# Kernel tuning notes

Hardware: AMD Instinct MI355X
Metric: run time of the kernel (lower is better)

The kernel has to match this reference:

```python
import jax, jax.numpy as jnp
import numpy as np

B, S, DIM, EXTRA, NK, NH, NL = 16, 256, 41, 1, 128, 4, 3
ND = DIM + EXTRA  # 42 channels after appending the Time2Vec extra channel


def _lin(key, fin, fout):
    kw, kb = jax.random.split(key)
    w = jax.random.normal(kw, (fin, fout), jnp.float32) / np.float32(np.sqrt(fin))
    b = jax.random.normal(kb, (fout,), jnp.float32) * 0.01
    return w, b


def _stack(key, fin, fout):
    ws, bs = zip(*[_lin(k, fin, fout) for k in jax.random.split(key, NL)])
    return jnp.stack(ws), jnp.stack(bs)


def setup_inputs():
    key = jax.random.key(0)
    ks = jax.random.split(key, 32)
    inp = {}
    inp['context_x'] = jnp.sort(jax.random.uniform(ks[0], (B, S), jnp.float32), axis=1)
    inp['value'] = jax.random.normal(ks[1], (B, S, DIM), jnp.float32)
    mask = (jax.random.uniform(ks[2], (B, S, DIM)) < 0.23).astype(jnp.float32)
    inp['mask'] = mask
    inp['target_value'] = jax.random.normal(ks[3], (B, S, DIM), jnp.float32)
    inp['target_mask'] = mask * (jax.random.uniform(ks[4], (B, S, DIM)) < 0.3).astype(jnp.float32)
    inp['t2v_w0'] = jax.random.normal(ks[5], (1,), jnp.float32)
    inp['t2v_b0'] = jax.random.normal(ks[6], (1,), jnp.float32)
    inp['edge_w'], inp['edge_b'] = _lin(ks[7], 2, NK)
    inp['chan_w'], inp['chan_b'] = _lin(ks[8], ND, NK)
    inp['time_w'], inp['time_b'] = _lin(ks[9], 1, NK)
    base = 10
    for pre, dk in (('ct', 2 * NK), ('tc', 2 * NK), ('ca', NK)):
        inp[pre + '_wq'], inp[pre + '_bq'] = _stack(ks[base], NK, NK); base += 1
        inp[pre + '_wk'], inp[pre + '_bk'] = _stack(ks[base], dk, NK); base += 1
        inp[pre + '_wv'], inp[pre + '_bv'] = _stack(ks[base], dk, NK); base += 1
        inp[pre + '_wo'], inp[pre + '_bo'] = _stack(ks[base], NK, NK); base += 1
    inp['en_w'], inp['en_b'] = _stack(ks[base], 3 * NK, NK); base += 1
    inp['out_w'], inp['out_b'] = _lin(ks[base], 3 * NK, 1)
    return inp


def _mab2(Q, K, wq, bq, wk, bk, wv, bv, wo, bo, mask):
    # GraFITi MAB2: fc_q/fc_k/fc_v -> dim_out, multihead attn, O = Q + A@V, then O += relu(fc_o(O))
    q = Q @ wq + bq
    k = K @ wk + bk
    v = K @ wv + bv
    b, nq, d = q.shape
    dh = d // NH
    qh = q.reshape(b, nq, NH, dh)
    kh = k.reshape(b, -1, NH, dh)
    vh = v.reshape(b, -1, NH, dh)
    att = jnp.einsum('bqhd,bkhd->bhqk', qh, kh) / np.float32(np.sqrt(d))
    if mask is not None:
        att = jnp.where(mask[:, None] == 0, jnp.float32(-1e10), att)
    A = jax.nn.softmax(att, axis=-1)
    o = (qh + jnp.einsum('bhqk,bkhd->bqhd', A, vh)).reshape(b, nq, d)
    return o + jax.nn.relu(o @ wo + bo)


def _forward(context_x, value, mask, target_value, target_mask, t2v_w0, t2v_b0,
             edge_w, edge_b, chan_w, chan_b, time_w, time_b,
             ct_wq, ct_bq, ct_wk, ct_bk, ct_wv, ct_bv, ct_wo, ct_bo,
             tc_wq, tc_bq, tc_wk, tc_bk, tc_wv, tc_bv, tc_wo, tc_bo,
             en_w, en_b,
             ca_wq, ca_bq, ca_wk, ca_bk, ca_wv, ca_bv, ca_wo, ca_bo,
             out_w, out_b):
    te = (t2v_w0 * context_x + t2v_b0)[:, :, None]  # Time2Vec linear channel [B,S,1]
    value_f = jnp.concatenate([value, te], -1)  # [B,S,ND]
    mask_f = jnp.concatenate([mask, jnp.ones((B, S, EXTRA), jnp.float32)], -1)
    tval_f = jnp.concatenate([target_value, te], -1)
    tmask_f = jnp.concatenate([target_mask, jnp.zeros((B, S, EXTRA), jnp.float32)], -1)
    # ragged compaction: observed entries first, zero-padded to the batch max count
    full_len = int(np.asarray(jnp.max(jnp.sum(mask_f, axis=(1, 2)))))
    order = jnp.argsort(-mask_f.reshape(B, -1), axis=1, stable=True)[:, :full_len]
    take = lambda x: jnp.take_along_axis(x.reshape(B, -1), order, axis=1)
    mk_ = take(mask_f)  # [B,L]: ones then zero padding
    U_val = take(value_f) * mk_
    target_U_ = take(tval_f) * mk_
    target_mask_ = take(tmask_f) * mk_
    mki = mk_.astype(jnp.int32)
    T_inds_ = take(jnp.broadcast_to(jnp.arange(S, dtype=jnp.int32)[None, :, None], (B, S, ND))) * mki
    C_inds_ = take(jnp.broadcast_to(jnp.arange(ND, dtype=jnp.int32)[None, None, :], (B, S, ND))) * mki
    C_mask = (C_inds_[:, None, :] == jnp.arange(ND)[None, :, None]).astype(jnp.float32) * mk_[:, None, :]
    T_mask = (T_inds_[:, None, :] == jnp.arange(S)[None, :, None]).astype(jnp.float32) * mk_[:, None, :]
    U_ind = 1.0 - mk_ + target_mask_
    U = jax.nn.relu(jnp.stack([U_val, U_ind], -1) @ edge_w + edge_b) * mk_[:, :, None]  # [B,L,NK]
    T_ = jnp.sin(context_x[:, :, None] @ time_w + time_b)  # [B,S,NK]
    # one_hot(arange(ND)) @ chan_w == chan_w
    C_ = jnp.broadcast_to(jax.nn.relu(chan_w + chan_b)[None], (B, ND, NK))
    gT = lambda x, idx: jnp.take_along_axis(x, jnp.broadcast_to(idx[:, :, None], (B, full_len, NK)), axis=1)
    for i in range(NL):
        k_t = gT(T_, T_inds_)
        C2 = _mab2(C_, jnp.concatenate([k_t, U], -1), ct_wq[i], ct_bq[i], ct_wk[i], ct_bk[i], ct_wv[i], ct_bv[i], ct_wo[i], ct_bo[i], C_mask)
        k_c = gT(C_, C_inds_)
        T2 = _mab2(T_, jnp.concatenate([k_c, U], -1), tc_wq[i], tc_bq[i], tc_wk[i], tc_bk[i], tc_wv[i], tc_bv[i], tc_wo[i], tc_bo[i], T_mask)
        U = jax.nn.relu(U + jnp.concatenate([U, k_t, k_c], -1) @ en_w[i] + en_b[i]) * mk_[:, :, None]
        C_ = _mab2(C2, C2, ca_wq[i], ca_bq[i], ca_wk[i], ca_bk[i], ca_wv[i], ca_bv[i], ca_wo[i], ca_bo[i], None)
        T_ = T2
    k_t = gT(T_, T_inds_)
    k_c = gT(C_, C_inds_)
    output = jnp.concatenate([U, k_t, k_c], -1) @ out_w + out_b  # [B,L,1]
    return output, target_U_, target_mask_


def reference(context_x, value, mask, target_value, target_mask, t2v_w0, t2v_b0, edge_w, edge_b, chan_w, chan_b, time_w, time_b, ct_wq, ct_bq, ct_wk, ct_bk, ct_wv, ct_bv, ct_wo, ct_bo, tc_wq, tc_bq, tc_wk, tc_bk, tc_wv, tc_bv, tc_wo, tc_bo, en_w, en_b, ca_wq, ca_bq, ca_wk, ca_bk, ca_wv, ca_bv, ca_wo, ca_bo, out_w, out_b):
    return _forward(context_x, value, mask, target_value, target_mask, t2v_w0, t2v_b0, edge_w, edge_b, chan_w, chan_b, time_w, time_b, ct_wq, ct_bq, ct_wk, ct_bk, ct_wv, ct_bv, ct_wo, ct_bo, tc_wq, tc_bq, tc_wk, tc_bk, tc_wv, tc_bv, tc_wo, tc_bo, en_w, en_b, ca_wq, ca_bq, ca_wk, ca_bk, ca_wv, ca_bv, ca_wo, ca_bo, out_w, out_b)
```

## Files before the change

### kernel.cpp

```cpp
#include <hip/hip_runtime.h>
#include <math.h>

#define NB   16
#define SS   256
#define DIMV 41
#define NDV  42
#define NKD  128
#define NHD  4
#define DH   32
#define NLAY 3
#define TOT  (SS*NDV)
#define NCH  42

typedef __attribute__((ext_vector_type(8))) short short8;
typedef __attribute__((ext_vector_type(4))) float floatx4;

__device__ __forceinline__ short f2bf(float x) {
    unsigned u = __float_as_uint(x);
    u += 0x7fff + ((u >> 16) & 1);
    return (short)(u >> 16);
}
__device__ __forceinline__ float bfs2f(short s) {
    return __uint_as_float(((unsigned)(unsigned short)s) << 16);
}
__device__ __forceinline__ float bf2f(unsigned s) {
    return __uint_as_float(s << 16);
}

struct Seg { const short* ptr; const int* ind; int ns; };

__device__ __forceinline__ const short* seg_row(const Seg s, int gm, int Lb) {
    if (s.ind) {
        int b = gm / Lb;
        int id = s.ind[gm]; if (id < 0) id = 0;
        return s.ptr + ((size_t)b * s.ns + (size_t)id) * NKD;
    }
    return s.ptr + (size_t)gm * NKD;
}


__device__ __forceinline__ void compactA_body(int bx, const float* __restrict__ maskp,
                                              int* __restrict__ chunkcnt)
{
    const int b = bx / NCH, ch = bx % NCH;
    const int tid = threadIdx.x;
    const int idx = ch * 256 + tid;
    const int s = idx / NDV, c = idx % NDV;
    float m = (c < DIMV) ? maskp[((size_t)b*SS + s)*DIMV + c] : 1.0f;
    int x = (m != 0.0f) ? 1 : 0;
    #pragma unroll
    for (int off = 32; off; off >>= 1) x += __shfl_down(x, off);
    __shared__ int ws4[4];
    if ((tid & 63) == 0) ws4[tid >> 6] = x;
    __syncthreads();
    if (tid == 0) chunkcnt[bx] = ws4[0] + ws4[1] + ws4[2] + ws4[3];
}

__device__ __forceinline__ void zero_body(int bx, int* __restrict__ lo_t,
                                          int* __restrict__ hi_t)
{
    int i = bx*256 + threadIdx.x;
    if (i < NB*SS) { lo_t[i] = 0; hi_t[i] = 0; }
}

__device__ __forceinline__ void initT_body(int bx, const float* __restrict__ cx,
                                           const float* __restrict__ tw,
                                           const float* __restrict__ tb,
                                           short* __restrict__ T)
{
    int i = bx * 256 + threadIdx.x;
    if (i >= NB*SS*16) return;
    int row = i >> 4;
    int k = (i & 15) << 3;
    float t = cx[row];
    short8 r;
    #pragma unroll
    for (int j = 0; j < 8; j++) r[j] = f2bf(sinf(t*tw[k+j] + tb[k+j]));
    *(short8*)(T + (size_t)row*NKD + k) = r;
}

__device__ __forceinline__ void initC_body(int bx, const float* __restrict__ cw,
                                           const float* __restrict__ cb,
                                           short* __restrict__ C)
{
    int i = bx * 256 + threadIdx.x;
    if (i >= NB*NDV*16) return;
    int row = i >> 4;
    int c = row % NDV;
    int k = (i & 15) << 3;
    short8 r;
    #pragma unroll
    for (int j = 0; j < 8; j++) r[j] = f2bf(fmaxf(cw[(size_t)c*NKD + k+j] + cb[k+j], 0.f));
    *(short8*)(C + (size_t)row*NKD + k) = r;
}

template<int Kg>
__device__ __forceinline__ void prep1(const float* __restrict__ src,
                                      short* __restrict__ dst, int rel)
{
    const int per = Kg*128;
    int i = rel / per; int r2 = rel - i*per;
    int n = r2 / Kg;   int k = r2 - n*Kg;
    dst[rel] = f2bf(src[(size_t)i*per + (size_t)k*128 + n]);
}

#define W_TOTAL 933888
__device__ __forceinline__ void prepw_body(int bx,
    const float* ctq, const float* ctk, const float* ctv, const float* cto,
    const float* tcq, const float* tck, const float* tcv, const float* tco,
    const float* caq, const float* cak, const float* cav, const float* cao,
    const float* enw, short* __restrict__ arena)
{
    int idx = bx*256 + threadIdx.x;
    if (idx >= W_TOTAL) return;
    if      (idx < 49152 ) prep1<128>(ctq, arena + 0,      idx - 0);
    else if (idx < 147456) prep1<256>(ctk, arena + 49152,  idx - 49152);
    else if (idx < 245760) prep1<256>(ctv, arena + 147456, idx - 147456);
    else if (idx < 294912) prep1<128>(cto, arena + 245760, idx - 245760);
    else if (idx < 344064) prep1<128>(tcq, arena + 294912, idx - 294912);
    else if (idx < 442368) prep1<256>(tck, arena + 344064, idx - 344064);
    else if (idx < 540672) prep1<256>(tcv, arena + 442368, idx - 442368);
    else if (idx < 589824) prep1<128>(tco, arena + 540672, idx - 540672);
    else if (idx < 638976) prep1<128>(caq, arena + 589824, idx - 589824);
    else if (idx < 688128) prep1<128>(cak, arena + 638976, idx - 638976);
    else if (idx < 737280) prep1<128>(cav, arena + 688128, idx - 688128);
    else if (idx < 786432) prep1<128>(cao, arena + 737280, idx - 737280);
    else                   prep1<384>(enw, arena + 786432, idx - 786432);
}

__device__ __forceinline__ void trange_body(int bx, const int* __restrict__ tind,
                                            int* __restrict__ lo_t,
                                            int* __restrict__ hi_t, int L)
{
    int p = bx*256 + threadIdx.x;
    if (p >= NB*L) return;
    int b = p / L, l = p - b*L;
    int t = tind[p];
    if (t < 0) return;
    int tp = (l > 0) ? tind[p-1] : -999;
    int tn = (l+1 < L) ? tind[p+1] : -999;
    if (tp != t) lo_t[b*SS + t] = l;
    if (tn != t) hi_t[b*SS + t] = l+1;
}

__device__ __forceinline__ void cperm_body(int b, const int* __restrict__ cind,
                                           int* __restrict__ invp,
                                           int* __restrict__ clo,
                                           int* __restrict__ chi, int L)
{
    __shared__ int hist[NDV];
    __shared__ int base[NDV];
    __shared__ int padc, cntsh;
    const int tid = threadIdx.x;
    if (tid < NDV) hist[tid] = 0;
    if (tid == 0) padc = 0;
    __syncthreads();
    for (int l = tid; l < L; l += 256) {
        int c = cind[(size_t)b*L + l];
        if (c >= 0) atomicAdd(&hist[c], 1);
    }
    __syncthreads();
    if (tid == 0) {
        int run = 0;
        for (int c = 0; c < NDV; c++) {
            base[c] = run; clo[b*NDV + c] = run;
            run += hist[c]; chi[b*NDV + c] = run;
        }
        cntsh = run;
    }
    __syncthreads();
    if (tid < NDV) hist[tid] = 0;
    __syncthreads();
    const int cnt = cntsh;
    for (int l = tid; l < L; l += 256) {
        int c = cind[(size_t)b*L + l];
        int pos;
        if (c >= 0) pos = base[c] + atomicAdd(&hist[c], 1);
        else        pos = cnt + atomicAdd(&padc, 1);
        invp[(size_t)b*L + l] = b*L + pos;
    }
}

__device__ __forceinline__ void initU_body(int bx, const float* __restrict__ uval,
                                           const float* __restrict__ uind,
                                           const float* __restrict__ mkb,
                                           const float* __restrict__ ew,
                                           const float* __restrict__ eb,
                                           short* __restrict__ U, int BL)
{
    int i = bx * 256 + threadIdx.x;
    if (i >= BL*16) return;
    int row = i >> 4;
    int k = (i & 15) << 3;
    float uv = uval[row], ui = uind[row], m = mkb[row];
    short8 r;
    #pragma unroll
    for (int j = 0; j < 8; j++)
        r[j] = f2bf(fmaxf(uv*ew[k+j] + ui*ew[NKD+k+j] + eb[k+j], 0.f) * m);
    *(short8*)(U + (size_t)row*NKD + k) = r;
}

template<int NSEG, int MODE>
__device__ __forceinline__ void mgemm_body(char* smem, int bx,
           Seg s0, Seg s1, Seg s2, const short* __restrict__ Wt,
           const float* __restrict__ bias, short* __restrict__ D,
           int M, int Lb, const float* __restrict__ mkp)
{
    short (*As)[40] = (short (*)[40])smem;
    short (*Bs)[40] = (short (*)[40])(smem + 10240);
    const int bm = bx * 128;
    const int tid = threadIdx.x;
    const int wv = tid >> 6;
    const int lane = tid & 63;
    const int quad = lane >> 4;
    const int l16 = lane & 15;
    const int K = NSEG * 128;
    floatx4 acc[2][8];
    #pragma unroll
    for (int i = 0; i < 2; i++)
        #pragma unroll
        for (int j = 0; j < 8; j++) acc[i][j] = (floatx4){0.f,0.f,0.f,0.f};

    const int arow = tid >> 1;
    const int acol = (tid & 1) * 16;
    int gmc = bm + arow; if (gmc > M-1) gmc = M-1;
    const short* rowp0 = seg_row(s0, gmc, Lb);
    const short* rowp1 = (NSEG > 1) ? seg_row(s1, gmc, Lb) : nullptr;
    const short* rowp2 = (NSEG > 2) ? seg_row(s2, gmc, Lb) : nullptr;

    for (int k0 = 0; k0 < K; k0 += 32) {
        {
            const short* rp;
            if (NSEG == 1) rp = rowp0;
            else if (NSEG == 2) rp = (k0 < 128) ? rowp0 : rowp1;
            else rp = (k0 < 128) ? rowp0 : ((k0 < 256) ? rowp1 : rowp2);
            const int ks = k0 & 127;
            const short* src = rp + ks + acol;
            *(short8*)&As[arow][acol]   = *(const short8*)(src);
            *(short8*)&As[arow][acol+8] = *(const short8*)(src+8);
        }
        {
            const short* src = Wt + (size_t)arow*K + k0 + acol;
            *(short8*)&Bs[arow][acol]   = *(const short8*)(src);
            *(short8*)&Bs[arow][acol+8] = *(const short8*)(src+8);
        }
        __syncthreads();
        short8 af0 = *(short8*)&As[wv*32 + l16][quad*8];
        short8 af1 = *(short8*)&As[wv*32 + 16 + l16][quad*8];
        #pragma unroll
        for (int nf = 0; nf < 8; nf++) {
            short8 bf = *(short8*)&Bs[nf*16 + l16][quad*8];
            acc[0][nf] = __builtin_amdgcn_mfma_f32_16x16x32_bf16(af0, bf, acc[0][nf], 0, 0, 0);
            acc[1][nf] = __builtin_amdgcn_mfma_f32_16x16x32_bf16(af1, bf, acc[1][nf], 0, 0, 0);
        }
        __syncthreads();
    }
    #pragma unroll
    for (int mf = 0; mf < 2; mf++) {
        #pragma unroll
        for (int r = 0; r < 4; r++) {
            int gm = bm + wv*32 + mf*16 + quad*4 + r;
            if (gm < M) {
                float mk = (MODE == 3) ? mkp[gm] : 0.f;
                const short* res = (MODE == 2 || MODE == 3) ? seg_row(s0, gm, Lb) : nullptr;
                #pragma unroll
                for (int nf = 0; nf < 8; nf++) {
                    int gn = nf*16 + l16;
                    float val = acc[mf][nf][r] + bias[gn];
                    if (MODE == 2) val = bfs2f(res[gn]) + fmaxf(val, 0.f);
                    else if (MODE == 3) val = fmaxf(bfs2f(res[gn]) + val, 0.f) * mk;
                    D[(size_t)gm*NKD + gn] = f2bf(val);
                }
            }
        }
    }
}

template<int NSEG, bool HASQ>
__device__ __forceinline__ void mgemm_kv_body(char* smem, int bx,
              Seg s0, Seg s1,
              const short* __restrict__ Wk, const float* __restrict__ bk,
              const short* __restrict__ Wv, const float* __restrict__ bv,
              const short* __restrict__ Wq, const float* __restrict__ bq,
              short* __restrict__ Qd,
              unsigned* __restrict__ KV, int M, int Lb, const int* __restrict__ rmap)
{
    short (*As)[40] = (short (*)[40])smem;
    short (*Bk_)[40] = (short (*)[40])(smem + 5120);
    short (*Bv_)[40] = (short (*)[40])(smem + 15360);
    short (*Bq_)[40] = (short (*)[40])(smem + 25600);
    const int bm = bx * 64;
    const int tid = threadIdx.x;
    const int wv = tid >> 6;
    const int lane = tid & 63;
    const int quad = lane >> 4;
    const int l16 = lane & 15;
    const int K = NSEG * 128;
    floatx4 acck[8], accv[8], accq[8];
    #pragma unroll
    for (int j = 0; j < 8; j++) {
        acck[j] = (floatx4){0.f,0.f,0.f,0.f};
        accv[j] = (floatx4){0.f,0.f,0.f,0.f};
        if (HASQ) accq[j] = (floatx4){0.f,0.f,0.f,0.f};
    }

    const int arow = tid >> 2;
    const int acol = (tid & 3) * 8;
    const int brow = tid >> 1;
    const int bcol = (tid & 1) * 16;
    int gmc = bm + arow; if (gmc > M-1) gmc = M-1;
    const short* rowp0 = seg_row(s0, gmc, Lb);
    const short* rowp1 = (NSEG > 1) ? seg_row(s1, gmc, Lb) : nullptr;

    for (int k0 = 0; k0 < K; k0 += 32) {
        {
            const short* rp = (NSEG == 1) ? rowp0 : ((k0 < 128) ? rowp0 : rowp1);
            const int ks = k0 & 127;
            *(short8*)&As[arow][acol] = *(const short8*)(rp + ks + acol);
        }
        {
            const short* sk = Wk + (size_t)brow*K + k0 + bcol;
            *(short8*)&Bk_[brow][bcol]   = *(const short8*)(sk);
            *(short8*)&Bk_[brow][bcol+8] = *(const short8*)(sk+8);
            const short* sv = Wv + (size_t)brow*K + k0 + bcol;
            *(short8*)&Bv_[brow][bcol]   = *(const short8*)(sv);
            *(short8*)&Bv_[brow][bcol+8] = *(const short8*)(sv+8);
            if (HASQ) {
                const short* sq = Wq + (size_t)brow*K + k0 + bcol;
                *(short8*)&Bq_[brow][bcol]   = *(const short8*)(sq);
                *(short8*)&Bq_[brow][bcol+8] = *(const short8*)(sq+8);
            }
        }
        __syncthreads();
        short8 af = *(short8*)&As[wv*16 + l16][quad*8];
        #pragma unroll
        for (int nf = 0; nf < 8; nf++) {
            short8 bfk = *(short8*)&Bk_[nf*16 + l16][quad*8];
            acck[nf] = __builtin_amdgcn_mfma_f32_16x16x32_bf16(af, bfk, acck[nf], 0, 0, 0);
            short8 bfv = *(short8*)&Bv_[nf*16 + l16][quad*8];
            accv[nf] = __builtin_amdgcn_mfma_f32_16x16x32_bf16(af, bfv, accv[nf], 0, 0, 0);
            if (HASQ) {
                short8 bfq = *(short8*)&Bq_[nf*16 + l16][quad*8];
                accq[nf] = __builtin_amdgcn_mfma_f32_16x16x32_bf16(af, bfq, accq[nf], 0, 0, 0);
            }
        }
        __syncthreads();
    }
    #pragma unroll
    for (int r = 0; r < 4; r++) {
        int gm = bm + wv*16 + quad*4 + r;
        if (gm < M) {
            int orow = rmap ? rmap[gm] : gm;
            #pragma unroll
            for (int nf = 0; nf < 8; nf++) {
                int gn = nf*16 + l16;
                float kf = acck[nf][r] + bk[gn];
                float vf = accv[nf][r] + bv[gn];
                unsigned pk = (unsigned)(unsigned short)f2bf(kf)
                            | ((unsigned)(unsigned short)f2bf(vf) << 16);
                KV[(size_t)orow*NKD + gn] = pk;
                if (HASQ) Qd[(size_t)gm*NKD + gn] = f2bf(accq[nf][r] + bq[gn]);
            }
        }
    }
}

template<int SPLIT>
__device__ __forceinline__ void sattn_body(int bx,
                  const short* __restrict__ q, const unsigned* __restrict__ kvb,
                  short* __restrict__ o, int nq, int nkv,
                  const int* __restrict__ lo_arr, const int* __restrict__ hi_arr)
{
    __shared__ float sm_m[4], sm_s[4], sm_a[4][DH];
    const int wvid = threadIdx.x >> 6;
    int gtask = bx * 4 + wvid;
    int task = gtask / SPLIT;
    int part = gtask % SPLIT;
    if (task >= NB * nq * NHD) return;
    const int h = task & 3;
    const int bq = task >> 2;
    const int qi = bq % nq;
    const int b = bq / nq;
    const int lane = threadIdx.x & 63;
    const int d = lane & 31;
    const int half = lane >> 5;
    int lo = lo_arr ? lo_arr[b*nq + qi] : 0;
    int hi = hi_arr ? hi_arr[b*nq + qi] : nkv;
    if (SPLIT == 2) {
        int mid = lo + ((hi - lo + 1) >> 1);
        if (part == 0) hi = mid; else lo = mid;
    }
    const float scale = 0.088388347648318447f;

    const float qv = bfs2f(q[((size_t)(b*nq + qi))*NKD + h*DH + d]);
    const unsigned* kb = kvb + (size_t)b*nkv*NKD + h*DH + d;

    float m = -INFINITY, ssum = 0.f, acc = 0.f;
    for (int l0 = lo; l0 < hi; l0 += 8) {
        unsigned ur[4];
        #pragma unroll
        for (int j = 0; j < 4; j++) {
            int l = l0 + 2*j + half;
            bool ok = (l < hi);
            ur[j] = ok ? kb[(size_t)l*NKD] : 0u;
        }
        #pragma unroll
        for (int j = 0; j < 4; j++) {
            int l = l0 + 2*j + half;
            float kr = bf2f(ur[j] & 0xffffu);
            float vr = bf2f(ur[j] >> 16);
            float partial = qv * kr;
            #pragma unroll
            for (int off = 16; off; off >>= 1) partial += __shfl_xor(partial, off);
            float s = partial * scale;
            if (l < hi) {
                float mn = fmaxf(m, s);
                float corr = __expf(m - mn);
                float p = __expf(s - mn);
                ssum = ssum * corr + p;
                acc  = acc  * corr + p * vr;
                m = mn;
            }
        }
    }
    float mo = __shfl_xor(m, 32);
    float M = fmaxf(m, mo);
    float corr = (m > -1e30f) ? __expf(m - M) : 0.f;
    ssum *= corr; acc *= corr;
    ssum += __shfl_xor(ssum, 32);
    acc  += __shfl_xor(acc, 32);

    if (SPLIT == 1) {
        if (half == 0) {
            float res = (ssum > 0.f) ? acc / ssum : 0.f;
            o[((size_t)(b*nq + qi))*NKD + h*DH + d] = f2bf(qv + res);
        }
    } else {
        if (lane == 0) { sm_m[wvid] = M; sm_s[wvid] = ssum; }
        if (lane < DH) sm_a[wvid][lane] = acc;
        __syncthreads();
        if (part == 0 && lane < DH) {
            float m2 = sm_m[wvid+1], s2 = sm_s[wvid+1], a2 = sm_a[wvid+1][lane];
            float M2 = fmaxf(M, m2);
            float c1 = (M  > -1e30f) ? __expf(M  - M2) : 0.f;
            float c2 = (m2 > -1e30f) ? __expf(m2 - M2) : 0.f;
            float S = ssum * c1 + s2 * c2;
            float A = acc  * c1 + a2 * c2;
            float res = (S > 0.f) ? A / S : 0.f;
            float qv2 = bfs2f(q[((size_t)(b*nq + qi))*NKD + h*DH + lane]);
            o[((size_t)(b*nq + qi))*NKD + h*DH + lane] = f2bf(qv2 + res);
        }
    }
}


__global__ __launch_bounds__(256)
void k_pre1(const float* maskp, int* chunkcnt, int* lo_t, int* hi_t,
            const float* cx, const float* tw, const float* tb, short* T,
            const float* cw, const float* cb, short* C,
            const float* ctq, const float* ctk, const float* ctv, const float* cto,
            const float* tcq, const float* tck, const float* tcv, const float* tco,
            const float* caq, const float* cak, const float* cav, const float* cao,
            const float* enw, short* arena)
{
    int bx = blockIdx.x;
    if (bx < NB*NCH)            compactA_body(bx, maskp, chunkcnt);
    else if (bx < NB*NCH + 16)  zero_body(bx - NB*NCH, lo_t, hi_t);
    else if (bx < NB*NCH + 16 + 256) initT_body(bx - NB*NCH - 16, cx, tw, tb, T);
    else if (bx < NB*NCH + 16 + 256 + 42) initC_body(bx - NB*NCH - 16 - 256, cw, cb, C);
    else prepw_body(bx - NB*NCH - 16 - 256 - 42,
                    ctq, ctk, ctv, cto, tcq, tck, tcv, tco,
                    caq, cak, cav, cao, enw, arena);
}

__global__ __launch_bounds__(256)
void k_compactC(const float* __restrict__ cx, const float* __restrict__ value,
              const float* __restrict__ maskp, const float* __restrict__ tval,
              const float* __restrict__ tmaskp, const float* __restrict__ w0p,
              const float* __restrict__ b0p,
              const int* __restrict__ chunkcnt, int L,
              int* __restrict__ tind, int* __restrict__ cind,
              float* __restrict__ mkb, float* __restrict__ uval,
              float* __restrict__ uind,
              float* __restrict__ outTU, float* __restrict__ outTM)
{
    const int blk = blockIdx.x;
    const int b = blk / NCH, ch = blk % NCH;
    const int tid = threadIdx.x, lane = tid & 63, wv = tid >> 6;
    const int idx = ch * 256 + tid;
    const int s = idx / NDV, c = idx % NDV;
    float mval = (c < DIMV) ? maskp[((size_t)b*SS + s)*DIMV + c] : 1.0f;
    int m = (mval != 0.0f) ? 1 : 0;
    int x = m;
    #pragma unroll
    for (int off = 1; off < 64; off <<= 1) {
        int y = __shfl_up(x, off);
        if (lane >= off) x += y;
    }
    __shared__ int wsum[4];
    __shared__ int s_off, s_cnt;
    if (lane == 63) wsum[wv] = x;
    if (tid < 64) {
        int v2 = (tid < NCH) ? chunkcnt[b*NCH + tid] : 0;
        int x2 = v2;
        #pragma unroll
        for (int off = 1; off < 64; off <<= 1) {
            int y2 = __shfl_up(x2, off);
            if (tid >= off) x2 += y2;
        }
        if (tid == ch) s_off = x2 - v2;
        if (tid == 63) s_cnt = x2;
    }
    __syncthreads();
    int wbase = 0;
    for (int w = 0; w < wv; w++) wbase += wsum[w];
    const int excl = x - m + wbase;
    const int vbefore = s_off + excl;
    const int cnt = s_cnt;
    const int pos = m ? vbefore : (cnt + (idx - vbefore));
    if (pos < L) {
        const float w0 = w0p[0], b0 = b0p[0];
        float te = w0 * cx[(size_t)b*SS + s] + b0;
        float vf, tvf, tmf;
        if (c < DIMV) {
            size_t o = ((size_t)b*SS + s)*DIMV + c;
            vf = value[o]; tvf = tval[o]; tmf = tmaskp[o];
        } else { vf = te; tvf = te; tmf = 0.0f; }
        size_t p = (size_t)b*L + pos;
        if (m) {
            tind[p] = s; cind[p] = c; mkb[p] = 1.0f;
            uval[p] = vf; uind[p] = tmf;
            outTU[p] = tvf; outTM[p] = tmf;
        } else {
            tind[p] = -1; cind[p] = -1; mkb[p] = 0.0f;
            uval[p] = 0.0f; uind[p] = 1.0f;
            outTU[p] = 0.0f; outTM[p] = 0.0f;
        }
    }
}

__global__ __launch_bounds__(256)
void k_pre4(const int* tind, int* lo_t, int* hi_t, int L, int gTr,
            const int* cind, int* invp, int* clo, int* chi,
            const float* uval, const float* uind, const float* mkb,
            const float* ew, const float* eb, short* U, int BL)
{
    int bx = blockIdx.x;
    if (bx < gTr) trange_body(bx, tind, lo_t, hi_t, L);
    else if (bx < gTr + NB) cperm_body(bx - gTr, cind, invp, clo, chi, L);
    else initU_body(bx - gTr - NB, uval, uind, mkb, ew, eb, U, BL);
}

__global__ __launch_bounds__(256)
void k_phase1(int g0, int g1, int g2,
              const short* T1, const int* tind, const short* U,
              const short* wkct, const float* bkct, const short* wvct, const float* bvct,
              unsigned* KVct, const int* invp,
              const short* C1, const short* wqct, const float* bqct, short* qC,
              const int* cind,
              const short* wktc, const float* bktc, const short* wvtc, const float* bvtc,
              unsigned* KVtc,
              const short* wqtc, const float* bqtc, short* qT,
              int BL, int L)
{
    __shared__ __align__(16) char smem[25600];
    int bx = blockIdx.x;
    if (bx < g0) {
        mgemm_kv_body<2,false>(smem, bx, Seg{T1,tind,SS}, Seg{U,nullptr,0},
            wkct, bkct, wvct, bvct, nullptr, nullptr, nullptr, KVct, BL, L, invp);
    } else if (bx < g0+g1) {
        mgemm_body<1,0>(smem, bx-g0, Seg{C1,nullptr,0}, Seg{nullptr,nullptr,0},
            Seg{nullptr,nullptr,0}, wqct, bqct, qC, NB*NDV, 1, nullptr);
    } else if (bx < g0+g1+g2) {
        mgemm_kv_body<2,false>(smem, bx-g0-g1, Seg{C1,cind,NDV}, Seg{U,nullptr,0},
            wktc, bktc, wvtc, bvtc, nullptr, nullptr, nullptr, KVtc, BL, L, nullptr);
    } else {
        mgemm_body<1,0>(smem, bx-g0-g1-g2, Seg{T1,nullptr,0}, Seg{nullptr,nullptr,0},
            Seg{nullptr,nullptr,0}, wqtc, bqtc, qT, NB*SS, 1, nullptr);
    }
}

__global__ __launch_bounds__(256)
void k_phase2(int g0, const short* qC, const unsigned* KVct, short* oC,
              const int* clo, const int* chi, int L,
              const short* qT, const unsigned* KVtc, short* oT,
              const int* lo_t, const int* hi_t)
{
    int bx = blockIdx.x;
    if (bx < g0) sattn_body<2>(bx, qC, KVct, oC, NDV, L, clo, chi);
    else         sattn_body<1>(bx-g0, qT, KVtc, oT, SS, L, lo_t, hi_t);
}

__global__ __launch_bounds__(256)
void k_phase3(int g0, int g1,
              const short* oC, const short* woct, const float* boct, short* C2,
              const short* oT, const short* wotc, const float* botc, short* T2b,
              const short* U, const short* T1, const int* tind,
              const short* C1, const int* cind,
              const short* wen, const float* ben, short* Unew, const float* mkb,
              int BL, int L)
{
    __shared__ __align__(16) char smem[20480];
    int bx = blockIdx.x;
    if (bx < g0)
        mgemm_body<1,2>(smem, bx, Seg{oC,nullptr,0}, Seg{nullptr,nullptr,0},
            Seg{nullptr,nullptr,0}, woct, boct, C2, NB*NDV, 1, nullptr);
    else if (bx < g0+g1)
        mgemm_body<1,2>(smem, bx-g0, Seg{oT,nullptr,0}, Seg{nullptr,nullptr,0},
            Seg{nullptr,nullptr,0}, wotc, botc, T2b, NB*SS, 1, nullptr);
    else
        mgemm_body<3,3>(smem, bx-g0-g1, Seg{U,nullptr,0}, Seg{T1,tind,SS},
            Seg{C1,cind,NDV}, wen, ben, Unew, BL, L, mkb);
}

__global__ __launch_bounds__(256)
void k_ca_kvq(const short* C2, const short* wk, const float* bk,
              const short* wv, const float* bv, const short* wq, const float* bq,
              short* qC, unsigned* KV)
{
    __shared__ __align__(16) char smem[35840];
    mgemm_kv_body<1,true>(smem, blockIdx.x, Seg{C2,nullptr,0}, Seg{nullptr,nullptr,0},
                          wk, bk, wv, bv, wq, bq, qC, KV, NB*NDV, 1, nullptr);
}

__global__ __launch_bounds__(256)
void k_ca_attn(const short* qC, const unsigned* kv, short* oC)
{
    sattn_body<2>(blockIdx.x, qC, kv, oC, NDV, NDV, nullptr, nullptr);
}

__global__ __launch_bounds__(256)
void k_ca_oproj(const short* oC, const short* wo, const float* bo, short* C1)
{
    __shared__ __align__(16) char smem[20480];
    mgemm_body<1,2>(smem, blockIdx.x, Seg{oC,nullptr,0}, Seg{nullptr,nullptr,0},
                    Seg{nullptr,nullptr,0}, wo, bo, C1, NB*NDV, 1, nullptr);
}

__global__ __launch_bounds__(256)
void k_out(const short* __restrict__ U, const short* __restrict__ T1,
           const short* __restrict__ C1, const int* __restrict__ tind,
           const int* __restrict__ cind, const float* __restrict__ ow,
           const float* __restrict__ obp, float* __restrict__ out,
           int BL, int L)
{
    int row = blockIdx.x * 4 + (threadIdx.x >> 6);
    int lane = threadIdx.x & 63;
    if (row >= BL) return;
    int b = row / L;
    int ti = tind[row]; if (ti < 0) ti = 0;
    int ci = cind[row]; if (ci < 0) ci = 0;
    const short* u = U + (size_t)row*NKD;
    const short* a = T1 + ((size_t)(b*SS + ti))*NKD;
    const short* c = C1 + ((size_t)(b*NDV + ci))*NKD;
    float s = bfs2f(u[lane])*ow[lane]     + bfs2f(u[lane+64])*ow[lane+64]
            + bfs2f(a[lane])*ow[128+lane] + bfs2f(a[lane+64])*ow[192+lane]
            + bfs2f(c[lane])*ow[256+lane] + bfs2f(c[lane+64])*ow[320+lane];
    #pragma unroll
    for (int off = 32; off; off >>= 1) s += __shfl_down(s, off);
    if (lane == 0) out[row] = s + obp[0];
}

extern "C" void kernel_launch(void* const* d_in, const int* in_sizes, int n_in,
                              void* d_out, int out_size, void* d_ws, size_t ws_size,
                              hipStream_t stream)
{
    const float* cx     = (const float*)d_in[0];
    const float* value  = (const float*)d_in[1];
    const float* maskp  = (const float*)d_in[2];
    const float* tval   = (const float*)d_in[3];
    const float* tmaskp = (const float*)d_in[4];
    const float* w0     = (const float*)d_in[5];
    const float* b0     = (const float*)d_in[6];
    const float* edge_w = (const float*)d_in[7];
    const float* edge_b = (const float*)d_in[8];
    const float* chan_w = (const float*)d_in[9];
    const float* chan_b = (const float*)d_in[10];
    const float* time_w = (const float*)d_in[11];
    const float* time_b = (const float*)d_in[12];
    const float* ct_wq = (const float*)d_in[13];
    const float* ct_bq = (const float*)d_in[14];
    const float* ct_wk = (const float*)d_in[15];
    const float* ct_bk = (const float*)d_in[16];
    const float* ct_wv = (const float*)d_in[17];
    const float* ct_bv = (const float*)d_in[18];
    const float* ct_wo = (const float*)d_in[19];
    const float* ct_bo = (const float*)d_in[20];
    const float* tc_wq = (const float*)d_in[21];
    const float* tc_bq = (const float*)d_in[22];
    const float* tc_wk = (const float*)d_in[23];
    const float* tc_bk = (const float*)d_in[24];
    const float* tc_wv = (const float*)d_in[25];
    const float* tc_bv = (const float*)d_in[26];
    const float* tc_wo = (const float*)d_in[27];
    const float* tc_bo = (const float*)d_in[28];
    const float* ca_wq = (const float*)d_in[29];
    const float* ca_bq = (const float*)d_in[30];
    const float* ca_wk = (const float*)d_in[31];
    const float* ca_bk = (const float*)d_in[32];
    const float* ca_wv = (const float*)d_in[33];
    const float* ca_bv = (const float*)d_in[34];
    const float* ca_wo = (const float*)d_in[35];
    const float* ca_bo = (const float*)d_in[36];
    const float* en_w  = (const float*)d_in[37];
    const float* en_b  = (const float*)d_in[38];
    const float* out_w = (const float*)d_in[39];
    const float* out_b = (const float*)d_in[40];

    const int BL = out_size / 3;
    const int L  = BL / NB;

    char* p = (char*)d_ws;
    auto alloc = [&](size_t n) { char* r = p; p += (n + 255) & ~(size_t)255; return r; };
    int*      tind   = (int*)  alloc((size_t)BL*4);
    int*      cind   = (int*)  alloc((size_t)BL*4);
    float*    mkb    = (float*)alloc((size_t)BL*4);
    float*    uval   = (float*)alloc((size_t)BL*4);
    float*    uind   = (float*)alloc((size_t)BL*4);
    int*      lo_t   = (int*)  alloc((size_t)NB*SS*4);
    int*      hi_t   = (int*)  alloc((size_t)NB*SS*4);
    int*      clo    = (int*)  alloc((size_t)NB*NDV*4);
    int*      chi    = (int*)  alloc((size_t)NB*NDV*4);
    int*      invp   = (int*)  alloc((size_t)BL*4);
    int*      chunkc = (int*)  alloc((size_t)NB*NCH*4);
    short*    waren  = (short*)alloc((size_t)W_TOTAL*2);
    short*    U    = (short*)alloc((size_t)BL*NKD*2);
    short*    Unew = (short*)alloc((size_t)BL*NKD*2);
    unsigned* KVct = (unsigned*)alloc((size_t)BL*NKD*4);
    unsigned* KVtc = (unsigned*)alloc((size_t)BL*NKD*4);
    unsigned* kvCa = (unsigned*)alloc((size_t)NB*NDV*NKD*4);
    short*    T1   = (short*)alloc((size_t)NB*SS*NKD*2);
    short*    T2b  = (short*)alloc((size_t)NB*SS*NKD*2);
    short*    qT   = (short*)alloc((size_t)NB*SS*NKD*2);
    short*    oT   = (short*)alloc((size_t)NB*SS*NKD*2);
    short*    C1   = (short*)alloc((size_t)NB*NDV*NKD*2);
    short*    C2   = (short*)alloc((size_t)NB*NDV*NKD*2);
    short*    qC   = (short*)alloc((size_t)NB*NDV*NKD*2);
    short*    oC   = (short*)alloc((size_t)NB*NDV*NKD*2);

    float* outMain = (float*)d_out;
    float* outTU = outMain + BL;
    float* outTM = outMain + 2*BL;

    const size_t OCTQ=0, OCTK=49152, OCTV=147456, OCTO=245760;
    const size_t OTCQ=294912, OTCK=344064, OTCV=442368, OTCO=540672;
    const size_t OCAQ=589824, OCAK=638976, OCAV=688128, OCAO=737280, OEN=786432;

    k_pre1<<<NB*NCH + 16 + 256 + 42 + W_TOTAL/256, 256, 0, stream>>>(
        maskp, chunkc, lo_t, hi_t, cx, time_w, time_b, T1, chan_w, chan_b, C1,
        ct_wq, ct_wk, ct_wv, ct_wo, tc_wq, tc_wk, tc_wv, tc_wo,
        ca_wq, ca_wk, ca_wv, ca_wo, en_w, waren);
    k_compactC<<<NB*NCH, 256, 0, stream>>>(cx, value, maskp, tval, tmaskp, w0, b0,
                                           chunkc, L, tind, cind, mkb, uval, uind,
                                           outTU, outTM);
    {
        const int gTr = (NB*L + 255)/256;
        const int gU  = (BL*16 + 255)/256;
        k_pre4<<<gTr + NB + gU, 256, 0, stream>>>(
            tind, lo_t, hi_t, L, gTr, cind, invp, clo, chi,
            uval, uind, mkb, edge_w, edge_b, U, BL);
    }

    const int gBL  = (BL + 127)/128;
    const int gKV  = (BL + 63)/64;
    const int gC   = (NB*NDV + 127)/128;
    const int gT   = (NB*SS + 127)/128;
    const int gCa  = (NB*NDV + 63)/64;
    const int aC2  = NB*NDV*NHD*2/4;
    const int aTC  = NB*SS*NHD/4;

    for (int i = 0; i < NLAY; i++) {
        const size_t bOff = (size_t)i*NKD;
        const short* wq_ct = waren + OCTQ + (size_t)i*128*128;
        const short* wk_ct = waren + OCTK + (size_t)i*256*128;
        const short* wv_ct = waren + OCTV + (size_t)i*256*128;
        const short* wo_ct = waren + OCTO + (size_t)i*128*128;
        const short* wq_tc = waren + OTCQ + (size_t)i*128*128;
        const short* wk_tc = waren + OTCK + (size_t)i*256*128;
        const short* wv_tc = waren + OTCV + (size_t)i*256*128;
        const short* wo_tc = waren + OTCO + (size_t)i*128*128;
        const short* wq_ca = waren + OCAQ + (size_t)i*128*128;
        const short* wk_ca = waren + OCAK + (size_t)i*128*128;
        const short* wv_ca = waren + OCAV + (size_t)i*128*128;
        const short* wo_ca = waren + OCAO + (size_t)i*128*128;
        const short* w_en  = waren + OEN  + (size_t)i*384*128;

        k_phase1<<<gKV + gC + gKV + gT, 256, 0, stream>>>(
            gKV, gC, gKV,
            T1, tind, U,
            wk_ct, ct_bk + bOff, wv_ct, ct_bv + bOff, KVct, invp,
            C1, wq_ct, ct_bq + bOff, qC,
            cind, wk_tc, tc_bk + bOff, wv_tc, tc_bv + bOff, KVtc,
            wq_tc, tc_bq + bOff, qT, BL, L);
        k_phase2<<<aC2 + aTC, 256, 0, stream>>>(
            aC2, qC, KVct, oC, clo, chi, L, qT, KVtc, oT, lo_t, hi_t);
        k_phase3<<<gC + gT + gBL, 256, 0, stream>>>(
            gC, gT, oC, wo_ct, ct_bo + bOff, C2, oT, wo_tc, tc_bo + bOff, T2b,
            U, T1, tind, C1, cind, w_en, en_b + bOff, Unew, mkb, BL, L);
        k_ca_kvq<<<gCa, 256, 0, stream>>>(C2, wk_ca, ca_bk + bOff,
            wv_ca, ca_bv + bOff, wq_ca, ca_bq + bOff, qC, kvCa);
        k_ca_attn<<<aC2, 256, 0, stream>>>(qC, kvCa, oC);
        k_ca_oproj<<<gC, 256, 0, stream>>>(oC, wo_ca, ca_bo + bOff, C1);

        short* t = U;  U = Unew; Unew = t;
        t = T1; T1 = T2b; T2b = t;
    }

    k_out<<<(BL + 3)/4, 256, 0, stream>>>(U, T1, C1, tind, cind,
                                          out_w, out_b, outMain, BL, L);
}
```

Measured before the change: 465.3 us.

## Fuse channel output projection with cross-attention QKV projections in phase3

Merges the ct output projection (C2 = oC + relu(oC·Wo + b)) and the following ca Q/K/V projections into one block routine. C2 is kept in shared memory instead of being written to global memory and read back by a separate k_ca_kvq launch. This removes one kernel launch per layer plus the C2 global round trip. In exchange, phase3 needs more shared memory, and the fused blocks run three projections one after another, so those blocks do more serial work. The block count for this part changes to gCa.

```diff
diff --git a/kernel.cpp b/kernel.cpp
--- a/kernel.cpp
+++ b/kernel.cpp
@@ -276,19 +276,16 @@
     }
 }
 
-template<int NSEG, bool HASQ>
+template<int NSEG>
 __device__ __forceinline__ void mgemm_kv_body(char* smem, int bx,
               Seg s0, Seg s1,
               const short* __restrict__ Wk, const float* __restrict__ bk,
               const short* __restrict__ Wv, const float* __restrict__ bv,
-              const short* __restrict__ Wq, const float* __restrict__ bq,
-              short* __restrict__ Qd,
               unsigned* __restrict__ KV, int M, int Lb, const int* __restrict__ rmap)
 {
     short (*As)[40] = (short (*)[40])smem;
     short (*Bk_)[40] = (short (*)[40])(smem + 5120);
     short (*Bv_)[40] = (short (*)[40])(smem + 15360);
-    short (*Bq_)[40] = (short (*)[40])(smem + 25600);
     const int bm = bx * 64;
     const int tid = threadIdx.x;
     const int wv = tid >> 6;
@@ -296,12 +293,11 @@
     const int quad = lane >> 4;
     const int l16 = lane & 15;
     const int K = NSEG * 128;
-    floatx4 acck[8], accv[8], accq[8];
+    floatx4 acck[8], accv[8];
     #pragma unroll
     for (int j = 0; j < 8; j++) {
         acck[j] = (floatx4){0.f,0.f,0.f,0.f};
         accv[j] = (floatx4){0.f,0.f,0.f,0.f};
-        if (HASQ) accq[j] = (floatx4){0.f,0.f,0.f,0.f};
     }
 
     const int arow = tid >> 2;
@@ -325,11 +321,6 @@
             const short* sv = Wv + (size_t)brow*K + k0 + bcol;
             *(short8*)&Bv_[brow][bcol]   = *(const short8*)(sv);
             *(short8*)&Bv_[brow][bcol+8] = *(const short8*)(sv+8);
-            if (HASQ) {
-                const short* sq = Wq + (size_t)brow*K + k0 + bcol;
-                *(short8*)&Bq_[brow][bcol]   = *(const short8*)(sq);
-                *(short8*)&Bq_[brow][bcol+8] = *(const short8*)(sq+8);
-            }
         }
         __syncthreads();
         short8 af = *(short8*)&As[wv*16 + l16][quad*8];
@@ -339,10 +330,6 @@
             acck[nf] = __builtin_amdgcn_mfma_f32_16x16x32_bf16(af, bfk, acck[nf], 0, 0, 0);
             short8 bfv = *(short8*)&Bv_[nf*16 + l16][quad*8];
             accv[nf] = __builtin_amdgcn_mfma_f32_16x16x32_bf16(af, bfv, accv[nf], 0, 0, 0);
-            if (HASQ) {
-                short8 bfq = *(short8*)&Bq_[nf*16 + l16][quad*8];
-                accq[nf] = __builtin_amdgcn_mfma_f32_16x16x32_bf16(af, bfq, accq[nf], 0, 0, 0);
-            }
         }
         __syncthreads();
     }
@@ -359,7 +346,116 @@
                 unsigned pk = (unsigned)(unsigned short)f2bf(kf)
                             | ((unsigned)(unsigned short)f2bf(vf) << 16);
                 KV[(size_t)orow*NKD + gn] = pk;
-                if (HASQ) Qd[(size_t)gm*NKD + gn] = f2bf(accq[nf][r] + bq[gn]);
+            }
+        }
+    }
+}
+
+__device__ __forceinline__ void octca_body(char* smem, int bx,
+    const short* __restrict__ oC,
+    const short* __restrict__ wo, const float* __restrict__ bo,
+    const short* __restrict__ wq, const float* __restrict__ bq,
+    const short* __restrict__ wk, const float* __restrict__ bk,
+    const short* __restrict__ wv, const float* __restrict__ bv,
+    short* __restrict__ qC, unsigned* __restrict__ KV, int M)
+{
+    short (*C2t)[136] = (short (*)[136])smem;
+    short (*Bs)[40]   = (short (*)[40])(smem + 17408);
+    short (*As)[40]   = (short (*)[40])(smem + 27648);
+    const int bm = bx * 64;
+    const int tid = threadIdx.x;
+    const int wv_ = tid >> 6;
+    const int lane = tid & 63;
+    const int quad = lane >> 4;
+    const int l16 = lane & 15;
+    const int arow = tid >> 2;
+    const int acol = (tid & 3) * 8;
+    const int brow = tid >> 1;
+    const int bcol = (tid & 1) * 16;
+    int gmc = bm + arow; if (gmc > M-1) gmc = M-1;
+    const short* rowp = oC + (size_t)gmc * NKD;
+
+    floatx4 acc[8];
+    #pragma unroll
+    for (int j = 0; j < 8; j++) acc[j] = (floatx4){0.f,0.f,0.f,0.f};
+    for (int k0 = 0; k0 < 128; k0 += 32) {
+        *(short8*)&As[arow][acol] = *(const short8*)(rowp + k0 + acol);
+        const short* sw = wo + (size_t)brow*128 + k0 + bcol;
+        *(short8*)&Bs[brow][bcol]   = *(const short8*)(sw);
+        *(short8*)&Bs[brow][bcol+8] = *(const short8*)(sw+8);
+        __syncthreads();
+        short8 af = *(short8*)&As[wv_*16 + l16][quad*8];
+        #pragma unroll
+        for (int nf = 0; nf < 8; nf++) {
+            short8 bf = *(short8*)&Bs[nf*16 + l16][quad*8];
+            acc[nf] = __builtin_amdgcn_mfma_f32_16x16x32_bf16(af, bf, acc[nf], 0, 0, 0);
+        }
+        __syncthreads();
+    }
+    #pragma unroll
+    for (int r = 0; r < 4; r++) {
+        int lrow = wv_*16 + quad*4 + r;
+        int gm = bm + lrow; int gmr = (gm > M-1) ? (M-1) : gm;
+        const short* res = oC + (size_t)gmr*NKD;
+        #pragma unroll
+        for (int nf = 0; nf < 8; nf++) {
+            int gn = nf*16 + l16;
+            float val = acc[nf][r] + bo[gn];
+            val = bfs2f(res[gn]) + fmaxf(val, 0.f);
+            C2t[lrow][gn] = f2bf(val);
+        }
+    }
+    __syncthreads();
+
+    floatx4 acck[8];
+    for (int proj = 0; proj < 3; proj++) {
+        const short* W = (proj == 0) ? wq : ((proj == 1) ? wk : wv);
+        floatx4 a2[8];
+        #pragma unroll
+        for (int j = 0; j < 8; j++) a2[j] = (floatx4){0.f,0.f,0.f,0.f};
+        for (int k0 = 0; k0 < 128; k0 += 32) {
+            const short* sw = W + (size_t)brow*128 + k0 + bcol;
+            *(short8*)&Bs[brow][bcol]   = *(const short8*)(sw);
+            *(short8*)&Bs[brow][bcol+8] = *(const short8*)(sw+8);
+            __syncthreads();
+            short8 af = *(short8*)&C2t[wv_*16 + l16][k0 + quad*8];
+            #pragma unroll
+            for (int nf = 0; nf < 8; nf++) {
+                short8 bf = *(short8*)&Bs[nf*16 + l16][quad*8];
+                a2[nf] = __builtin_amdgcn_mfma_f32_16x16x32_bf16(af, bf, a2[nf], 0, 0, 0);
+            }
+            __syncthreads();
+        }
+        if (proj == 0) {
+            #pragma unroll
+            for (int r = 0; r < 4; r++) {
+                int gm = bm + wv_*16 + quad*4 + r;
+                if (gm < M) {
+                    #pragma unroll
+                    for (int nf = 0; nf < 8; nf++) {
+                        int gn = nf*16 + l16;
+                        qC[(size_t)gm*NKD + gn] = f2bf(a2[nf][r] + bq[gn]);
+                    }
+                }
+            }
+        } else if (proj == 1) {
+            #pragma unroll
+            for (int j = 0; j < 8; j++) acck[j] = a2[j];
+        } else {
+            #pragma unroll
+            for (int r = 0; r < 4; r++) {
+                int gm = bm + wv_*16 + quad*4 + r;
+                if (gm < M) {
+                    #pragma unroll
+                    for (int nf = 0; nf < 8; nf++) {
+                        int gn = nf*16 + l16;
+                        float kf = acck[nf][r] + bk[gn];
+                        float vf = a2[nf][r] + bv[gn];
+                        KV[(size_t)gm*NKD + gn] =
+                            (unsigned)(unsigned short)f2bf(kf)
+                          | ((unsigned)(unsigned short)f2bf(vf) << 16);
+                    }
+                }
             }
         }
     }
@@ -566,14 +662,14 @@
     __shared__ __align__(16) char smem[25600];
     int bx = blockIdx.x;
     if (bx < g0) {
-        mgemm_kv_body<2,false>(smem, bx, Seg{T1,tind,SS}, Seg{U,nullptr,0},
-            wkct, bkct, wvct, bvct, nullptr, nullptr, nullptr, KVct, BL, L, invp);
+        mgemm_kv_body<2>(smem, bx, Seg{T1,tind,SS}, Seg{U,nullptr,0},
+            wkct, bkct, wvct, bvct, KVct, BL, L, invp);
     } else if (bx < g0+g1) {
         mgemm_body<1,0>(smem, bx-g0, Seg{C1,nullptr,0}, Seg{nullptr,nullptr,0},
             Seg{nullptr,nullptr,0}, wqct, bqct, qC, NB*NDV, 1, nullptr);
     } else if (bx < g0+g1+g2) {
-        mgemm_kv_body<2,false>(smem, bx-g0-g1, Seg{C1,cind,NDV}, Seg{U,nullptr,0},
-            wktc, bktc, wvtc, bvtc, nullptr, nullptr, nullptr, KVtc, BL, L, nullptr);
+        mgemm_kv_body<2>(smem, bx-g0-g1, Seg{C1,cind,NDV}, Seg{U,nullptr,0},
+            wktc, bktc, wvtc, bvtc, KVtc, BL, L, nullptr);
     } else {
         mgemm_body<1,0>(smem, bx-g0-g1-g2, Seg{T1,nullptr,0}, Seg{nullptr,nullptr,0},
             Seg{nullptr,nullptr,0}, wqtc, bqtc, qT, NB*SS, 1, nullptr);
@@ -593,34 +689,28 @@
 
 __global__ __launch_bounds__(256)
 void k_phase3(int g0, int g1,
-              const short* oC, const short* woct, const float* boct, short* C2,
+              const short* oC, const short* woct, const float* boct,
+              const short* wq_ca, const float* bq_ca,
+              const short* wk_ca, const float* bk_ca,
+              const short* wv_ca, const float* bv_ca,
+              short* qC, unsigned* kvCa,
               const short* oT, const short* wotc, const float* botc, short* T2b,
               const short* U, const short* T1, const int* tind,
               const short* C1, const int* cind,
               const short* wen, const float* ben, short* Unew, const float* mkb,
               int BL, int L)
 {
-    __shared__ __align__(16) char smem[20480];
+    __shared__ __align__(16) char smem[32768];
     int bx = blockIdx.x;
     if (bx < g0)
-        mgemm_body<1,2>(smem, bx, Seg{oC,nullptr,0}, Seg{nullptr,nullptr,0},
-            Seg{nullptr,nullptr,0}, woct, boct, C2, NB*NDV, 1, nullptr);
+        octca_body(smem, bx, oC, woct, boct, wq_ca, bq_ca, wk_ca, bk_ca,
+                   wv_ca, bv_ca, qC, kvCa, NB*NDV);
     else if (bx < g0+g1)
         mgemm_body<1,2>(smem, bx-g0, Seg{oT,nullptr,0}, Seg{nullptr,nullptr,0},
             Seg{nullptr,nullptr,0}, wotc, botc, T2b, NB*SS, 1, nullptr);
     else
         mgemm_body<3,3>(smem, bx-g0-g1, Seg{U,nullptr,0}, Seg{T1,tind,SS},
             Seg{C1,cind,NDV}, wen, ben, Unew, BL, L, mkb);
-}
-
-__global__ __launch_bounds__(256)
-void k_ca_kvq(const short* C2, const short* wk, const float* bk,
-              const short* wv, const float* bv, const short* wq, const float* bq,
-              short* qC, unsigned* KV)
-{
-    __shared__ __align__(16) char smem[35840];
-    mgemm_kv_body<1,true>(smem, blockIdx.x, Seg{C2,nullptr,0}, Seg{nullptr,nullptr,0},
-                          wk, bk, wv, bv, wq, bq, qC, KV, NB*NDV, 1, nullptr);
 }
 
 __global__ __launch_bounds__(256)
@@ -734,7 +824,6 @@
     short*    qT   = (short*)alloc((size_t)NB*SS*NKD*2);
     short*    oT   = (short*)alloc((size_t)NB*SS*NKD*2);
     short*    C1   = (short*)alloc((size_t)NB*NDV*NKD*2);
-    short*    C2   = (short*)alloc((size_t)NB*NDV*NKD*2);
     short*    qC   = (short*)alloc((size_t)NB*NDV*NKD*2);
     short*    oC   = (short*)alloc((size_t)NB*NDV*NKD*2);
 
@@ -794,11 +883,13 @@
             wq_tc, tc_bq + bOff, qT, BL, L);
         k_phase2<<<aC2 + aTC, 256, 0, stream>>>(
             aC2, qC, KVct, oC, clo, chi, L, qT, KVtc, oT, lo_t, hi_t);
-        k_phase3<<<gC + gT + gBL, 256, 0, stream>>>(
-            gC, gT, oC, wo_ct, ct_bo + bOff, C2, oT, wo_tc, tc_bo + bOff, T2b,
+        k_phase3<<<gCa + gT + gBL, 256, 0, stream>>>(
+            gCa, gT,
+            oC, wo_ct, ct_bo + bOff,
+            wq_ca, ca_bq + bOff, wk_ca, ca_bk + bOff, wv_ca, ca_bv + bOff,
+            qC, kvCa,
+            oT, wo_tc, tc_bo + bOff, T2b,
             U, T1, tind, C1, cind, w_en, en_b + bOff, Unew, mkb, BL, L);
-        k_ca_kvq<<<gCa, 256, 0, stream>>>(C2, wk_ca, ca_bk + bOff,
-            wv_ca, ca_bv + bOff, wq_ca, ca_bq + bOff, qC, kvCa);
         k_ca_attn<<<aC2, 256, 0, stream>>>(qC, kvCa, oC);
         k_ca_oproj<<<gC, 256, 0, stream>>>(oC, wo_ca, ca_bo + bOff, C1);
 
```

Result: faster. 453.0 us (-2.7%).
